# Performance work log

Measured on AMD Instinct MI355X. Metric: run time of the kernel, lower is better.

## Reference

```python
import jax, jax.numpy as jnp
import numpy as np

NUM_GRAPHS = 256  # fixed number of segments (batch.max()+1 in the torch code)

def setup_inputs() -> dict:
    key = jax.random.key(0)
    k1, k2, k3, k4, k5 = jax.random.split(key, 5)
    N, D, H = 200000, 256, 128
    x = jax.random.normal(k1, (N, D), dtype=jnp.float32)
    batch = jnp.sort(jax.random.randint(k2, (N,), 0, NUM_GRAPHS)).astype(jnp.int64)
    # attention MLP params: Linear(D->H), Tanh, Linear(H->1)
    w1 = jax.random.normal(k3, (D, H), dtype=jnp.float32) / np.sqrt(D)
    b1 = jnp.zeros((H,), dtype=jnp.float32)
    w2 = jax.random.normal(k4, (H, 1), dtype=jnp.float32) / np.sqrt(H)
    b2 = jnp.zeros((1,), dtype=jnp.float32)
    return {"x": x, "batch": batch, "w1": w1, "b1": b1, "w2": w2, "b2": b2}

def reference(x, batch, w1, b1, w2, b2):
    # attention scores: Linear -> tanh -> Linear -> [N,1]
    scores = jnp.tanh(x @ w1 + b1) @ w2 + b2          # [N,1]
    # NOTE: faithful to the original: softmax over ALL nodes (dim=0), not per-graph
    attn = jax.nn.softmax(scores, axis=0)              # [N,1]
    weighted = x * attn                                # [N,D]
    # masked per-graph sum == segment sum over graph ids
    out = jax.ops.segment_sum(weighted, batch, num_segments=NUM_GRAPHS)  # [B,D]
    return out
```

## Files before the change

### kernel.cpp

```cpp
#include <hip/hip_runtime.h>

#define NGRAPHS 256
#define DIM     256
#define HID     128
#define TILE    128
#define NPERS   512

typedef __attribute__((ext_vector_type(8))) short bf16x8;
typedef __attribute__((ext_vector_type(4))) float f32x4;

__device__ __forceinline__ ushort f2bf_rne(float f) {
    unsigned u = __float_as_uint(f);
    unsigned r = u + 0x7fffu + ((u >> 16) & 1u);
    return (ushort)(r >> 16);
}
__device__ __forceinline__ float tanh_fast(float x) {
    float e = __expf(2.0f * x);
    return 1.0f - 2.0f * __builtin_amdgcn_rcpf(1.0f + e);
}
__device__ __forceinline__ unsigned pack2(float a, float b) {
    unsigned ua = __float_as_uint(a), ub = __float_as_uint(b);
    unsigned ra = ua + 0x7fffu + ((ua >> 16) & 1u);
    unsigned rb = ub + 0x7fffu + ((ub >> 16) & 1u);
    return (ra >> 16) | (rb & 0xffff0000u);
}
__device__ __forceinline__ bf16x8 cvt8h(float4 v0, float4 v1) {
    union { unsigned w[4]; bf16x8 v; } H;
    H.w[0] = pack2(v0.x, v0.y);
    H.w[1] = pack2(v0.z, v0.w);
    H.w[2] = pack2(v1.x, v1.y);
    H.w[3] = pack2(v1.z, v1.w);
    return H.v;
}
__device__ __forceinline__ void glds16(const void* g, void* l) {
    __builtin_amdgcn_global_load_lds(
        (const __attribute__((address_space(1))) unsigned int*)g,
        (__attribute__((address_space(3))) unsigned int*)l, 16, 0, 0);
}

__global__ void k_prep(const float* __restrict__ w1, ushort* __restrict__ w1f)
{
    int idx = blockIdx.x * 256 + threadIdx.x;
    int k  = idx >> 7, nn = idx & 127;
    int ks = k >> 5, lhi = (k >> 3) & 3, j = k & 7;
    int nf = nn >> 4, llo = nn & 15;
    int lane = lhi * 16 + llo;
    w1f[(ks * 8 + nf) * 512 + lane * 8 + j] = f2bf_rne(w1[idx]);
}

__global__ __launch_bounds__(256, 2) void k_scores(
    const float* __restrict__ x, const int* __restrict__ batch,
    const ushort* __restrict__ w1f,
    const float* __restrict__ b1, const float* __restrict__ w2,
    const float* __restrict__ b2,
    float* __restrict__ wsp, float* __restrict__ wse, int* __restrict__ wsid,
    int n, int nblk)
{
    __shared__ __align__(16) ushort bs[DIM * HID];
    __shared__ float sred[4][2][DIM];
    __shared__ float evals[TILE];
    __shared__ int   gid[TILE];
    __shared__ float ep[4];

    const int t    = threadIdx.x;
    const int wid  = t >> 6;
    const int lane = t & 63;
    const int lhi  = lane >> 4;
    const int llo  = lane & 15;

#pragma unroll
    for (int i = 0; i < 16; ++i)
        glds16(w1f + (size_t)(i * 256 + t) * 8,
               (unsigned char*)bs + (i * 256 + wid * 64) * 16);
    asm volatile("s_waitcnt vmcnt(0)" ::: "memory");
    __builtin_amdgcn_s_barrier();

    float b2v = b2[0];
    float b1v[8], w2v[8];
#pragma unroll
    for (int nf = 0; nf < 8; ++nf) {
        b1v[nf] = b1[nf * 16 + llo];
        w2v[nf] = w2[nf * 16 + llo];
    }

    for (int tid = blockIdx.x; tid < nblk; tid += NPERS) {
        const int r0 = tid * TILE;

        if (t < TILE) {
            int r = r0 + t;
            gid[t] = batch[r < n ? r : (n - 1)];
        }

        int row0 = r0 + wid * 32 + llo;
        int row1 = row0 + 16;
        if (row0 >= n) row0 = n - 1;
        if (row1 >= n) row1 = n - 1;
        const float* xr0 = x + (size_t)row0 * DIM + lhi * 8;
        const float* xr1 = x + (size_t)row1 * DIM + lhi * 8;

        float4 pA[2][4];
        pA[0][0] = *(const float4*)(xr0);      pA[0][1] = *(const float4*)(xr0 + 4);
        pA[0][2] = *(const float4*)(xr1);      pA[0][3] = *(const float4*)(xr1 + 4);
        pA[1][0] = *(const float4*)(xr0 + 32); pA[1][1] = *(const float4*)(xr0 + 36);
        pA[1][2] = *(const float4*)(xr1 + 32); pA[1][3] = *(const float4*)(xr1 + 36);
        __builtin_amdgcn_sched_barrier(0);

        f32x4 acc[2][8];
#pragma unroll
        for (int i = 0; i < 2; ++i)
#pragma unroll
            for (int j = 0; j < 8; ++j) acc[i][j] = (f32x4){0.f, 0.f, 0.f, 0.f};

#pragma unroll
        for (int ks = 0; ks < 8; ++ks) {
            const int cur = ks & 1;
            bf16x8 ah0 = cvt8h(pA[cur][0], pA[cur][1]);
            bf16x8 ah1 = cvt8h(pA[cur][2], pA[cur][3]);
            if (ks + 2 < 8) {
                pA[cur][0] = *(const float4*)(xr0 + (ks + 2) * 32);
                pA[cur][1] = *(const float4*)(xr0 + (ks + 2) * 32 + 4);
                pA[cur][2] = *(const float4*)(xr1 + (ks + 2) * 32);
                pA[cur][3] = *(const float4*)(xr1 + (ks + 2) * 32 + 4);
            }
            __builtin_amdgcn_sched_barrier(0);
#pragma unroll
            for (int nf = 0; nf < 8; ++nf) {
                bf16x8 bh = *(const bf16x8*)&bs[ks * 4096 + nf * 512 + lane * 8];
                acc[0][nf] = __builtin_amdgcn_mfma_f32_16x16x32_bf16(ah0, bh, acc[0][nf], 0, 0, 0);
                acc[1][nf] = __builtin_amdgcn_mfma_f32_16x16x32_bf16(ah1, bh, acc[1][nf], 0, 0, 0);
            }
        }

        float4 xv0[16];
#pragma unroll
        for (int j = 0; j < 16; ++j) {
            int rsrc = r0 + wid * 32 + j;
            if (rsrc >= n) rsrc = n - 1;
            xv0[j] = *(const float4*)(x + (size_t)rsrc * DIM + lane * 4);
        }
        __builtin_amdgcn_sched_barrier(0);

        float sc[8];
#pragma unroll
        for (int mf = 0; mf < 2; ++mf)
#pragma unroll
            for (int rg = 0; rg < 4; ++rg) {
                float p = 0.f;
#pragma unroll
                for (int nf = 0; nf < 8; ++nf)
                    p += tanh_fast(acc[mf][nf][rg] + b1v[nf]) * w2v[nf];
                sc[mf * 4 + rg] = p;
            }
#pragma unroll
        for (int off = 1; off < 16; off <<= 1)
#pragma unroll
            for (int q = 0; q < 8; ++q) sc[q] += __shfl_xor(sc[q], off, 64);

        if (llo == 0) {
#pragma unroll
            for (int mf = 0; mf < 2; ++mf)
#pragma unroll
                for (int rg = 0; rg < 4; ++rg) {
                    int row = wid * 32 + mf * 16 + lhi * 4 + rg;
                    float s = sc[mf * 4 + rg] + b2v;
                    evals[row] = (r0 + row < n) ? __expf(s) : 0.f;
                }
        }
        __syncthreads();

        {
            float4 xv1[16];
#pragma unroll
            for (int j = 0; j < 16; ++j) {
                int rsrc = r0 + wid * 32 + 16 + j;
                if (rsrc >= n) rsrc = n - 1;
                xv1[j] = *(const float4*)(x + (size_t)rsrc * DIM + lane * 4);
            }
            __builtin_amdgcn_sched_barrier(0);

            const int g0 = gid[0];
            float4 a0 = {0.f, 0.f, 0.f, 0.f}, a1 = {0.f, 0.f, 0.f, 0.f};
#pragma unroll
            for (int j = 0; j < 16; ++j) {
                int row = wid * 32 + j;
                float e = evals[row];
                if (gid[row] != g0) {
                    a1.x = fmaf(e, xv0[j].x, a1.x); a1.y = fmaf(e, xv0[j].y, a1.y);
                    a1.z = fmaf(e, xv0[j].z, a1.z); a1.w = fmaf(e, xv0[j].w, a1.w);
                } else {
                    a0.x = fmaf(e, xv0[j].x, a0.x); a0.y = fmaf(e, xv0[j].y, a0.y);
                    a0.z = fmaf(e, xv0[j].z, a0.z); a0.w = fmaf(e, xv0[j].w, a0.w);
                }
            }
#pragma unroll
            for (int j = 0; j < 16; ++j) {
                int row = wid * 32 + 16 + j;
                float e = evals[row];
                if (gid[row] != g0) {
                    a1.x = fmaf(e, xv1[j].x, a1.x); a1.y = fmaf(e, xv1[j].y, a1.y);
                    a1.z = fmaf(e, xv1[j].z, a1.z); a1.w = fmaf(e, xv1[j].w, a1.w);
                } else {
                    a0.x = fmaf(e, xv1[j].x, a0.x); a0.y = fmaf(e, xv1[j].y, a0.y);
                    a0.z = fmaf(e, xv1[j].z, a0.z); a0.w = fmaf(e, xv1[j].w, a0.w);
                }
            }
            *(float4*)&sred[wid][0][lane * 4] = a0;
            *(float4*)&sred[wid][1][lane * 4] = a1;
        }
        __syncthreads();
        {
            float s0 = sred[0][0][t] + sred[1][0][t] + sred[2][0][t] + sred[3][0][t];
            float s1 = sred[0][1][t] + sred[1][1][t] + sred[2][1][t] + sred[3][1][t];
            wsp[(size_t)tid * 512 + t]       = s0;
            wsp[(size_t)tid * 512 + 256 + t] = s1;
            if (t == 0) wsid[tid] = gid[0];
        }

        float rsum = (t < TILE) ? evals[t] : 0.f;
#pragma unroll
        for (int off = 32; off; off >>= 1) rsum += __shfl_down(rsum, off, 64);
        if ((t & 63) == 0) ep[t >> 6] = rsum;
        __syncthreads();
        if (t == 0) wse[tid] = ep[0] + ep[1];
    }
}

__global__ __launch_bounds__(256) void k_combine(
    const int* __restrict__ batch, const float* __restrict__ wsp,
    const float* __restrict__ wse, const int* __restrict__ wsid,
    float* __restrict__ out, int n, int nblk)
{
    __shared__ float sred[256];
    __shared__ int bounds[2];
    const int g = blockIdx.x;
    const int d = threadIdx.x;

    float p = 0.f;
    for (int i = d; i < nblk; i += 256) p += wse[i];
    sred[d] = p;
    __syncthreads();
    for (int s = 128; s; s >>= 1) {
        if (d < s) sred[d] += sred[d + s];
        __syncthreads();
    }
    const float S = sred[0];

    if (d < 2) {
        int v = g + d;
        int lo = 0, hi = n;
        while (lo < hi) { int mid = (lo + hi) >> 1; if (batch[mid] < v) lo = mid + 1; else hi = mid; }
        bounds[d] = lo;
    }
    __syncthreads();

    const int st = bounds[0], en = bounds[1];
    float acc = 0.f;
    if (st < en) {
        for (int bb = st >> 7; bb <= (en - 1) >> 7; ++bb) {
            int slot = (wsid[bb] == g) ? 0 : 1;
            acc += wsp[(size_t)bb * 512 + slot * 256 + d];
        }
    }
    out[g * 256 + d] = acc / S;
}

extern "C" void kernel_launch(void* const* d_in, const int* in_sizes, int n_in,
                              void* d_out, int out_size, void* d_ws, size_t ws_size,
                              hipStream_t stream)
{
    const float* x     = (const float*)d_in[0];
    const int*   batch = (const int*)d_in[1];
    const float* w1    = (const float*)d_in[2];
    const float* b1    = (const float*)d_in[3];
    const float* w2    = (const float*)d_in[4];
    const float* b2    = (const float*)d_in[5];
    float* out = (float*)d_out;

    const int n    = in_sizes[1];
    const int nblk = (n + TILE - 1) / TILE;

    ushort* w1f = (ushort*)d_ws;
    float*  wsp = (float*)((char*)d_ws + (size_t)DIM * HID * sizeof(ushort));
    float*  wse = wsp + (size_t)nblk * 512;
    int*    wsid = (int*)(wse + nblk);

    k_prep<<<dim3(DIM * HID / 256), dim3(256), 0, stream>>>(w1, w1f);
    k_scores<<<dim3(NPERS), dim3(256), 0, stream>>>(x, batch, w1f,
                                                    b1, w2, b2, wsp, wse, wsid,
                                                    n, nblk);
    k_combine<<<dim3(NGRAPHS), dim3(256), 0, stream>>>(batch, wsp, wse, wsid,
                                                       out, n, nblk);
}
```

Measured before the change: 79.95 us.

## Make each wave own a 32-row group, removing block-level barriers

Each wavefront now handles an independent 32-row group instead of four waves sharing a 128-row tile. Graph-boundary detection uses a ballot over batch ids, and exp sums use wave shuffles. This removes all __syncthreads and the cross-wave shared-memory reduction. In exchange it writes four times as many partial rows to the workspace, so the write traffic and the reads in k_combine both grow.

```diff
diff --git a/kernel.cpp b/kernel.cpp
--- a/kernel.cpp
+++ b/kernel.cpp
@@ -3,7 +3,7 @@
 #define NGRAPHS 256
 #define DIM     256
 #define HID     128
-#define TILE    128
+#define GRP     32
 #define NPERS   512
 
 typedef __attribute__((ext_vector_type(8))) short bf16x8;
@@ -54,13 +54,10 @@
     const float* __restrict__ b1, const float* __restrict__ w2,
     const float* __restrict__ b2,
     float* __restrict__ wsp, float* __restrict__ wse, int* __restrict__ wsid,
-    int n, int nblk)
+    int n, int ngrp)
 {
     __shared__ __align__(16) ushort bs[DIM * HID];
-    __shared__ float sred[4][2][DIM];
-    __shared__ float evals[TILE];
-    __shared__ int   gid[TILE];
-    __shared__ float ep[4];
+    __shared__ float evw[4][GRP];
 
     const int t    = threadIdx.x;
     const int wid  = t >> 6;
@@ -75,7 +72,7 @@
     asm volatile("s_waitcnt vmcnt(0)" ::: "memory");
     __builtin_amdgcn_s_barrier();
 
-    float b2v = b2[0];
+    const float b2v = b2[0];
     float b1v[8], w2v[8];
 #pragma unroll
     for (int nf = 0; nf < 8; ++nf) {
@@ -83,16 +80,17 @@
         w2v[nf] = w2[nf * 16 + llo];
     }
 
-    for (int tid = blockIdx.x; tid < nblk; tid += NPERS) {
-        const int r0 = tid * TILE;
-
-        if (t < TILE) {
-            int r = r0 + t;
-            gid[t] = batch[r < n ? r : (n - 1)];
-        }
-
-        int row0 = r0 + wid * 32 + llo;
-        int row1 = row0 + 16;
+    for (int gq = blockIdx.x * 4 + wid; gq < ngrp; gq += NPERS * 4) {
+        const int r0 = gq * GRP;
+
+        int rb = r0 + (lane & 31); if (rb >= n) rb = n - 1;
+        int gv = batch[rb];
+        int g0 = __shfl(gv, 0, 64);
+        unsigned long long mb = __ballot(gv != g0);
+        int rtrans = mb ? (((int)__ffsll((long long)mb) - 1) & 31) : GRP;
+
+        int row0 = r0 + llo;
+        int row1 = r0 + 16 + llo;
         if (row0 >= n) row0 = n - 1;
         if (row1 >= n) row1 = n - 1;
         const float* xr0 = x + (size_t)row0 * DIM + lhi * 8;
@@ -134,7 +132,7 @@
         float4 xv0[16];
 #pragma unroll
         for (int j = 0; j < 16; ++j) {
-            int rsrc = r0 + wid * 32 + j;
+            int rsrc = r0 + j;
             if (rsrc >= n) rsrc = n - 1;
             xv0[j] = *(const float4*)(x + (size_t)rsrc * DIM + lane * 4);
         }
@@ -156,79 +154,74 @@
 #pragma unroll
             for (int q = 0; q < 8; ++q) sc[q] += __shfl_xor(sc[q], off, 64);
 
+        float e8[8];
+#pragma unroll
+        for (int mf = 0; mf < 2; ++mf)
+#pragma unroll
+            for (int rg = 0; rg < 4; ++rg) {
+                int row = mf * 16 + lhi * 4 + rg;
+                float s = sc[mf * 4 + rg] + b2v;
+                e8[mf * 4 + rg] = (r0 + row < n) ? __expf(s) : 0.f;
+            }
         if (llo == 0) {
 #pragma unroll
             for (int mf = 0; mf < 2; ++mf)
 #pragma unroll
-                for (int rg = 0; rg < 4; ++rg) {
-                    int row = wid * 32 + mf * 16 + lhi * 4 + rg;
-                    float s = sc[mf * 4 + rg] + b2v;
-                    evals[row] = (r0 + row < n) ? __expf(s) : 0.f;
-                }
-        }
-        __syncthreads();
-
-        {
-            float4 xv1[16];
-#pragma unroll
-            for (int j = 0; j < 16; ++j) {
-                int rsrc = r0 + wid * 32 + 16 + j;
-                if (rsrc >= n) rsrc = n - 1;
-                xv1[j] = *(const float4*)(x + (size_t)rsrc * DIM + lane * 4);
-            }
-            __builtin_amdgcn_sched_barrier(0);
-
-            const int g0 = gid[0];
-            float4 a0 = {0.f, 0.f, 0.f, 0.f}, a1 = {0.f, 0.f, 0.f, 0.f};
-#pragma unroll
-            for (int j = 0; j < 16; ++j) {
-                int row = wid * 32 + j;
-                float e = evals[row];
-                if (gid[row] != g0) {
-                    a1.x = fmaf(e, xv0[j].x, a1.x); a1.y = fmaf(e, xv0[j].y, a1.y);
-                    a1.z = fmaf(e, xv0[j].z, a1.z); a1.w = fmaf(e, xv0[j].w, a1.w);
-                } else {
-                    a0.x = fmaf(e, xv0[j].x, a0.x); a0.y = fmaf(e, xv0[j].y, a0.y);
-                    a0.z = fmaf(e, xv0[j].z, a0.z); a0.w = fmaf(e, xv0[j].w, a0.w);
-                }
-            }
-#pragma unroll
-            for (int j = 0; j < 16; ++j) {
-                int row = wid * 32 + 16 + j;
-                float e = evals[row];
-                if (gid[row] != g0) {
-                    a1.x = fmaf(e, xv1[j].x, a1.x); a1.y = fmaf(e, xv1[j].y, a1.y);
-                    a1.z = fmaf(e, xv1[j].z, a1.z); a1.w = fmaf(e, xv1[j].w, a1.w);
-                } else {
-                    a0.x = fmaf(e, xv1[j].x, a0.x); a0.y = fmaf(e, xv1[j].y, a0.y);
-                    a0.z = fmaf(e, xv1[j].z, a0.z); a0.w = fmaf(e, xv1[j].w, a0.w);
-                }
-            }
-            *(float4*)&sred[wid][0][lane * 4] = a0;
-            *(float4*)&sred[wid][1][lane * 4] = a1;
-        }
-        __syncthreads();
-        {
-            float s0 = sred[0][0][t] + sred[1][0][t] + sred[2][0][t] + sred[3][0][t];
-            float s1 = sred[0][1][t] + sred[1][1][t] + sred[2][1][t] + sred[3][1][t];
-            wsp[(size_t)tid * 512 + t]       = s0;
-            wsp[(size_t)tid * 512 + 256 + t] = s1;
-            if (t == 0) wsid[tid] = gid[0];
-        }
-
-        float rsum = (t < TILE) ? evals[t] : 0.f;
-#pragma unroll
-        for (int off = 32; off; off >>= 1) rsum += __shfl_down(rsum, off, 64);
-        if ((t & 63) == 0) ep[t >> 6] = rsum;
-        __syncthreads();
-        if (t == 0) wse[tid] = ep[0] + ep[1];
+                for (int rg = 0; rg < 4; ++rg)
+                    evw[wid][mf * 16 + lhi * 4 + rg] = e8[mf * 4 + rg];
+        }
+        asm volatile("s_waitcnt lgkmcnt(0)" ::: "memory");
+        __builtin_amdgcn_sched_barrier(0);
+
+        float esum = e8[0] + e8[1] + e8[2] + e8[3] + e8[4] + e8[5] + e8[6] + e8[7];
+        float tot = __shfl(esum, 0, 64) + __shfl(esum, 16, 64)
+                  + __shfl(esum, 32, 64) + __shfl(esum, 48, 64);
+        if (lane == 0) {
+            wse[gq]  = tot;
+            wsid[gq] = g0;
+        }
+
+        float4 xv1[16];
+#pragma unroll
+        for (int j = 0; j < 16; ++j) {
+            int rsrc = r0 + 16 + j;
+            if (rsrc >= n) rsrc = n - 1;
+            xv1[j] = *(const float4*)(x + (size_t)rsrc * DIM + lane * 4);
+        }
+        __builtin_amdgcn_sched_barrier(0);
+
+        float4 a0 = {0.f, 0.f, 0.f, 0.f}, a1 = {0.f, 0.f, 0.f, 0.f};
+#pragma unroll
+        for (int j = 0; j < 16; ++j) {
+            float e = evw[wid][j];
+            if (j < rtrans) {
+                a0.x = fmaf(e, xv0[j].x, a0.x); a0.y = fmaf(e, xv0[j].y, a0.y);
+                a0.z = fmaf(e, xv0[j].z, a0.z); a0.w = fmaf(e, xv0[j].w, a0.w);
+            } else {
+                a1.x = fmaf(e, xv0[j].x, a1.x); a1.y = fmaf(e, xv0[j].y, a1.y);
+                a1.z = fmaf(e, xv0[j].z, a1.z); a1.w = fmaf(e, xv0[j].w, a1.w);
+            }
+        }
+#pragma unroll
+        for (int j = 0; j < 16; ++j) {
+            float e = evw[wid][16 + j];
+            if (16 + j < rtrans) {
+                a0.x = fmaf(e, xv1[j].x, a0.x); a0.y = fmaf(e, xv1[j].y, a0.y);
+                a0.z = fmaf(e, xv1[j].z, a0.z); a0.w = fmaf(e, xv1[j].w, a0.w);
+            } else {
+                a1.x = fmaf(e, xv1[j].x, a1.x); a1.y = fmaf(e, xv1[j].y, a1.y);
+                a1.z = fmaf(e, xv1[j].z, a1.z); a1.w = fmaf(e, xv1[j].w, a1.w);
+            }
+        }
+        *(float4*)&wsp[(size_t)gq * 512 + lane * 4]       = a0;
+        *(float4*)&wsp[(size_t)gq * 512 + 256 + lane * 4] = a1;
     }
 }
 
 __global__ __launch_bounds__(256) void k_combine(
     const int* __restrict__ batch, const float* __restrict__ wsp,
     const float* __restrict__ wse, const int* __restrict__ wsid,
-    float* __restrict__ out, int n, int nblk)
+    float* __restrict__ out, int n, int ngrp)
 {
     __shared__ float sred[256];
     __shared__ int bounds[2];
@@ -236,7 +229,7 @@
     const int d = threadIdx.x;
 
     float p = 0.f;
-    for (int i = d; i < nblk; i += 256) p += wse[i];
+    for (int i = d; i < ngrp; i += 256) p += wse[i];
     sred[d] = p;
     __syncthreads();
     for (int s = 128; s; s >>= 1) {
@@ -256,7 +249,7 @@
     const int st = bounds[0], en = bounds[1];
     float acc = 0.f;
     if (st < en) {
-        for (int bb = st >> 7; bb <= (en - 1) >> 7; ++bb) {
+        for (int bb = st >> 5; bb <= (en - 1) >> 5; ++bb) {
             int slot = (wsid[bb] == g) ? 0 : 1;
             acc += wsp[(size_t)bb * 512 + slot * 256 + d];
         }
@@ -277,17 +270,17 @@
     float* out = (float*)d_out;
 
     const int n    = in_sizes[1];
-    const int nblk = (n + TILE - 1) / TILE;
+    const int ngrp = (n + GRP - 1) / GRP;
 
     ushort* w1f = (ushort*)d_ws;
     float*  wsp = (float*)((char*)d_ws + (size_t)DIM * HID * sizeof(ushort));
-    float*  wse = wsp + (size_t)nblk * 512;
-    int*    wsid = (int*)(wse + nblk);
+    float*  wse = wsp + (size_t)ngrp * 512;
+    int*    wsid = (int*)(wse + ngrp);
 
     k_prep<<<dim3(DIM * HID / 256), dim3(256), 0, stream>>>(w1, w1f);
     k_scores<<<dim3(NPERS), dim3(256), 0, stream>>>(x, batch, w1f,
                                                     b1, w2, b2, wsp, wse, wsid,
-                                                    n, nblk);
+                                                    n, ngrp);
     k_combine<<<dim3(NGRAPHS), dim3(256), 0, stream>>>(batch, wsp, wse, wsid,
-                                                       out, n, nblk);
-}
+                                                       out, n, ngrp);
+}
```

After: 90.77 us. 13.5% more time.
